# Kernel optimization log

Hardware: AMD Instinct MI355X
Metric: run time of the kernel (lower is better)

The kernel has to match this reference:

```python
import jax, jax.numpy as jnp
import numpy as np


def _ramp_filter(H):
    # skimage-style Fourier ramp filter: 2*|f| with f = fftfreq(H)
    f = np.fft.fftfreq(H)
    return (2.0 * np.abs(f)).astype(np.float32)


def setup_inputs() -> dict:
    key = jax.random.key(0)
    N, H_in, W_in, D_out = 8, 768, 360, 512
    radon_image = jax.random.normal(key, (N, 1, H_in, W_in), dtype=jnp.float32)
    hG = jnp.asarray(_ramp_filter(H_in)).reshape(1, 1, H_in, 1)
    return {"radon_image": radon_image, "hG": hG, "D_out": D_out}


def reference(radon_image, hG, D_out):
    N, _, H, W = radon_image.shape
    D = D_out
    # --- Fourier-domain ramp filtering (2D FFT, multiply by real filter along detector axis, real ifft) ---
    X = jnp.fft.fft2(radon_image[:, 0])                     # [N, H, W] complex
    h = hG[0, 0, :, 0]                                      # [H]
    filt = jnp.real(jnp.fft.ifft2(X * h[None, :, None])).astype(radon_image.dtype)  # [N, H, W]

    # --- backprojection grids (matches np.mgrid / tG construction) ---
    Xg, Yg = jnp.meshgrid(jnp.arange(D), jnp.arange(D), indexing="ij")
    xpr = (Xg - D // 2).astype(jnp.float32)
    ypr = (Yg - D // 2).astype(jnp.float32)
    th = (jnp.pi / 180.0) * jnp.linspace(0.0, 180.0, W, endpoint=False)  # [W]
    txs = -1.0 + jnp.arange(W, dtype=jnp.float32) * (2.0 / (W - 1))     # [W]

    hH = H // 2
    sy = (H - 1) / 2.0   # align_corners=True y scale
    sx = (W - 1) / 2.0   # align_corners=True x scale

    def body(recon, angle):
        th_i, tx_i = angle
        t = ypr * jnp.cos(th_i) - xpr * jnp.sin(th_i)       # [D, D]
        py = (t / hH + 1.0) * sy                            # pixel y coords [D, D]
        px = (tx_i + 1.0) * sx                              # scalar pixel x coord
        x0 = jnp.floor(px).astype(jnp.int32)
        wx = px - x0
        y0 = jnp.floor(py).astype(jnp.int32)
        wy = py - y0

        def samp_col(xi):
            vx = ((xi >= 0) & (xi < W)).astype(filt.dtype)
            col = filt[:, :, jnp.clip(xi, 0, W - 1)]        # [N, H]

            def samp_y(yi):
                vy = ((yi >= 0) & (yi < H)).astype(filt.dtype)
                return col[:, jnp.clip(yi, 0, H - 1)] * vy  # [N, D, D] zero-padded

            v = samp_y(y0) * (1.0 - wy) + samp_y(y0 + 1) * wy
            return v * vx

        val = samp_col(x0) * (1.0 - wx) + samp_col(x0 + 1) * wx  # [N, D, D]
        return recon + val, None

    recon0 = jnp.zeros((N, D, D), dtype=radon_image.dtype)
    recon, _ = jax.lax.scan(body, recon0, (th, txs))
    return (recon * (jnp.pi / (2.0 * W)))[:, None]          # [N, 1, D, D]
```

## Files before the change

kernel.cpp:

```cpp
#include <hip/hip_runtime.h>
#include <math.h>

#define N_IMG 8
#define H 768
#define W 360
#define D 512
#define SY 383.5f
#define SC 0.00436332312998582394f
#define NC 24
#define IPAD 384

typedef __fp16 h2 __attribute__((ext_vector_type(2)));
struct H2X2 { h2 a, b; };
typedef short short8 __attribute__((ext_vector_type(8)));
typedef float f32x4 __attribute__((ext_vector_type(4)));

__device__ inline unsigned bf16pair(float a, float b) {
    unsigned ua = __builtin_bit_cast(unsigned, a);
    unsigned ub = __builtin_bit_cast(unsigned, b);
    ua += 0x7FFFu + ((ua >> 16) & 1u);
    ub += 0x7FFFu + ((ub >> 16) & 1u);
    return (ua >> 16) | (ub & 0xFFFF0000u);
}

__global__ void build_g_kernel(const float* __restrict__ hG, float* __restrict__ g) {
    int m = blockIdx.x;
    int lane = threadIdx.x;
    float s = 0.f;
#pragma unroll
    for (int q = 0; q < 12; ++q) {
        int k = lane + 64 * q;
        int prod = (k * m) % H;
        float angr = (float)prod * 0.00818123086872313911f;
        s += hG[k] * cosf(angr);
    }
#pragma unroll
    for (int off = 32; off > 0; off >>= 1) s += __shfl_down(s, off);
    if (lane == 0) g[m] = s * (1.0f / (float)H);
}

#define KSTEPS 10

__global__ void build_angbg_kernel(const float* __restrict__ g, uint4* __restrict__ Bg,
                                   float2* __restrict__ ang) {
    int b = blockIdx.x;
    int t = threadIdx.x;
    if (b < 40) {
        int idx = b * 64 + t;
        int L  = idx & 63;
        int tj = idx >> 6;
        int nn = (tj & 3) * 16 + (L & 15);
        int kb = (tj >> 2) * 32 + (L >> 4) * 8;
        float bf[8];
#pragma unroll
        for (int s = 0; s < 8; ++s) {
            int d = nn + 128 - (kb + s);
            d += (d < 0) ? H : 0;
            bf[s] = g[d];
        }
        Bg[idx] = (uint4){bf16pair(bf[0], bf[1]), bf16pair(bf[2], bf[3]),
                          bf16pair(bf[4], bf[5]), bf16pair(bf[6], bf[7])};
    } else {
#pragma unroll
        for (int q = 0; q < 6; ++q) {
            int i = t + 64 * q;
            if (i < W) {
                float th = (float)i * 0.00872664625997164788f;
                float r = SY / 384.0f;
                ang[i] = make_float2(cosf(th) * r, -sinf(th) * r);
            }
        }
    }
}

__global__ __launch_bounds__(256)
void build_rc_kernel(const float* __restrict__ radon, uint4* __restrict__ rcC,
                     float4* __restrict__ out4) {
    __shared__ float xs[32][65];

    const int i0 = blockIdx.x * 64;
    const int c  = blockIdx.y;
    const int n  = blockIdx.z;
    const int tid = threadIdx.x;

    {
        int flat = ((n * NC) + c) * 6 + blockIdx.x;
        if (flat < 1024) {
            out4[flat * 512 + tid]       = make_float4(0.f, 0.f, 0.f, 0.f);
            out4[flat * 512 + 256 + tid] = make_float4(0.f, 0.f, 0.f, 0.f);
        }
    }

    {
        int mr    = tid >> 3;
        int lane8 = tid & 7;
        int ib = i0 + lane8 * 8;
        const float* src = radon + ((size_t)n * H + 32 * c + mr) * W + ib;
        float4 v0, v1;
        if (ib + 7 < W) {
            v0 = *(const float4*)src;
            v1 = *(const float4*)(src + 4);
        } else {
            v0 = make_float4(0.f, 0.f, 0.f, 0.f);
            v1 = make_float4(0.f, 0.f, 0.f, 0.f);
        }
        *(float4*)&xs[mr][lane8 * 8]     = v0;
        *(float4*)&xs[mr][lane8 * 8 + 4] = v1;
    }
    __syncthreads();

    const int il  = tid >> 2;
    const int oct = tid & 3;
    float v[8];
#pragma unroll
    for (int s = 0; s < 8; ++s) v[s] = xs[oct * 8 + s][il];
    uint4 pk = {bf16pair(v[0], v[1]), bf16pair(v[2], v[3]),
                bf16pair(v[4], v[5]), bf16pair(v[6], v[7])};
    rcC[(((size_t)n * NC + c) * IPAD + i0 + il) * 4 + oct] = pk;
}

__global__ __launch_bounds__(256)
void filt_gemm_kernel(const uint4* __restrict__ rcC, const uint4* __restrict__ Bg,
                      unsigned short* __restrict__ colp) {
    __shared__ _Float16 lx[16][64][4];

    const int grp = blockIdx.z;
    const int i0 = blockIdx.y * 16;
    const int y0 = blockIdx.x * 64;
    const int wv = threadIdx.x >> 6;
    const int L  = threadIdx.x & 63;

    const int c0 = (y0 / 32 + 20) % NC;
    const uint4* An = rcC + (size_t)(grp * 4 + wv) * NC * IPAD * 4;
    const int arow = i0 + (L & 15);
    const int aoff = L >> 4;

    f32x4 acc[4];
#pragma unroll
    for (int j = 0; j < 4; ++j) acc[j] = (f32x4){0.f, 0.f, 0.f, 0.f};

    for (int t = 0; t < KSTEPS; ++t) {
        int c = c0 + t;
        c -= (c >= NC) ? NC : 0;
        short8 a = __builtin_bit_cast(short8, An[((size_t)c * IPAD + arow) * 4 + aoff]);
#pragma unroll
        for (int j = 0; j < 4; ++j) {
            short8 b = __builtin_bit_cast(short8, Bg[(t * 4 + j) * 64 + L]);
            acc[j] = __builtin_amdgcn_mfma_f32_16x16x32_bf16(a, b, acc[j], 0, 0, 0);
        }
    }

#pragma unroll
    for (int j = 0; j < 4; ++j) {
#pragma unroll
        for (int r = 0; r < 4; ++r) {
            int ilc = (L >> 4) * 4 + r;
            int ylc = j * 16 + (L & 15);
            lx[ilc][ylc][wv] = (_Float16)(acc[j][r] * SC);
        }
    }
    __syncthreads();

    unsigned short* cp = colp + (size_t)grp * W * H * 4;
#pragma unroll
    for (int k = 0; k < 4; ++k) {
        int e = threadIdx.x + k * 256;
        int ilc = e >> 6, ylc = e & 63;
        int ig = i0 + ilc;
        if (ig < W) {
            uint2 v = *(const uint2*)&lx[ilc][ylc][0];
            *(uint2*)&cp[((size_t)ig * H + y0 + ylc) * 4] = v;
        }
    }
}

__global__ __launch_bounds__(512, 8)
void backproj_kernel(const unsigned short* __restrict__ colp,
                     const float2* __restrict__ angv, float* __restrict__ outb) {
    __shared__ __align__(16) H2X2 colh[2][H];

    const int bid = blockIdx.x;
    const int bz  = bid & 7;
    const int tle = bid >> 3;
    const int g  = bz >> 2;
    const int aq = bz & 3;
    const int a0 = aq * (W / 4);
    const int u0 = (tle >> 3) * 32;
    const int v0 = (tle & 7) * 64;
    const int tid = threadIdx.x;
    const int lane = tid & 63;
    const int tu = tid >> 6;

    const float vf = (float)(v0 + lane - D / 2);
    float uf[4];
#pragma unroll
    for (int r = 0; r < 4; ++r) uf[r] = (float)(u0 + tu + 8 * r - D / 2);

    const h2 hz = {(__fp16)0.f, (__fp16)0.f};
    float acc[4][4];
    h2 haccA[4], haccB[4];
#pragma unroll
    for (int r = 0; r < 4; ++r) {
#pragma unroll
        for (int nn = 0; nn < 4; ++nn) acc[r][nn] = 0.f;
        haccA[r] = hz;
        haccB[r] = hz;
    }

    const uint2* cp = (const uint2*)colp + (size_t)g * W * H;

    const int y1 = tid;
    const int y2 = tid + 512;

    {
        const int ab = a0 * H;
        colh[0][y1] = __builtin_bit_cast(H2X2, cp[ab + y1]);
        if (tid < 256) colh[0][y2] = __builtin_bit_cast(H2X2, cp[ab + y2]);
    }
    __syncthreads();

    for (int j = 0; j < W / 4; ++j) {
        int a = a0 + j;
        int an = (j + 1 < W / 4) ? (a + 1) : a;
        const int ab = an * H;
        uint2 d = cp[ab + y1];
        uint2 e = make_uint2(0u, 0u);
        if (tid < 256) e = cp[ab + y2];

        const int cb2 = j & 1;
        float2 AB = angv[a];
        float base = fmaf(vf, AB.x, SY);
#pragma unroll
        for (int r = 0; r < 4; ++r) {
            float py = fmaf(uf[r], AB.y, base);
            float wy = __builtin_amdgcn_fractf(py);
            int iy = (int)py;
            uint2 lo_raw = *(const uint2*)&colh[cb2][iy];
            uint2 hi_raw = *(const uint2*)&colh[cb2][iy + 1];
            H2X2 lo = __builtin_bit_cast(H2X2, lo_raw);
            H2X2 hi = __builtin_bit_cast(H2X2, hi_raw);
            h2 wy2 = __builtin_amdgcn_cvt_pkrtz(wy, wy);
            haccA[r] += lo.a + wy2 * (hi.a - lo.a);
            haccB[r] += lo.b + wy2 * (hi.b - lo.b);
        }

        if ((j & 15) == 15) {
#pragma unroll
            for (int r = 0; r < 4; ++r) {
                acc[r][0] += (float)haccA[r].x;
                acc[r][1] += (float)haccA[r].y;
                acc[r][2] += (float)haccB[r].x;
                acc[r][3] += (float)haccB[r].y;
                haccA[r] = hz;
                haccB[r] = hz;
            }
        }

        colh[cb2 ^ 1][y1] = __builtin_bit_cast(H2X2, d);
        if (tid < 256) colh[cb2 ^ 1][y2] = __builtin_bit_cast(H2X2, e);
        __syncthreads();
    }

#pragma unroll
    for (int r = 0; r < 4; ++r) {
        acc[r][0] += (float)haccA[r].x;
        acc[r][1] += (float)haccA[r].y;
        acc[r][2] += (float)haccB[r].x;
        acc[r][3] += (float)haccB[r].y;
        int u = u0 + tu + 8 * r;
#pragma unroll
        for (int nn = 0; nn < 4; ++nn) {
            size_t idx = ((size_t)(g * 4 + nn) * D + u) * D + v0 + lane;
            atomicAdd(&outb[idx], acc[r][nn]);
        }
    }
}

extern "C" void kernel_launch(void* const* d_in, const int* in_sizes, int n_in,
                              void* d_out, int out_size, void* d_ws, size_t ws_size,
                              hipStream_t stream) {
    const float* radon = (const float*)d_in[0];
    const float* hG    = (const float*)d_in[1];
    float* out = (float*)d_out;

    float*  g    = (float*)d_ws;
    float2* ang  = (float2*)((char*)d_ws + 4096);
    uint4*  Bg   = (uint4*)((char*)d_ws + 8192);
    unsigned short* colp = (unsigned short*)((char*)d_ws + 65536);
    uint4*  rcC  = (uint4*)((char*)d_ws + 4489216);

    build_g_kernel<<<H, 64, 0, stream>>>(hG, g);
    build_angbg_kernel<<<41, 64, 0, stream>>>(g, Bg, ang);
    build_rc_kernel<<<dim3(6, NC, N_IMG), 256, 0, stream>>>(radon, rcC, (float4*)out);
    filt_gemm_kernel<<<dim3(H / 64, 23, 2), 256, 0, stream>>>(rcC, Bg, colp);
    backproj_kernel<<<1024, 512, 0, stream>>>(colp, ang, out);
}
```

Before: 167.7 us.

## Interleave all 8 images per detector sample and split angles 8 ways in backprojection

The filtered sinogram layout changes from two groups of 4 images to a single interleaved 8-image row (16 bytes per detector bin), and the backprojection now processes all 8 images per block while splitting the angle range into 8 chunks instead of 4 images × 4 angle chunks. Each LDS lookup and bilinear weight computation is shared across 8 images rather than 4, which halves the per-image address/weight arithmetic and LDS instruction count. The cost is doubled LDS footprint (24 KB per block), more accumulator registers, a lowered occupancy hint (6 blocks), and twice as many atomic adds per block.

```diff
diff --git a/kernel.cpp b/kernel.cpp
--- a/kernel.cpp
+++ b/kernel.cpp
@@ -11,7 +11,6 @@
 #define IPAD 384
 
 typedef __fp16 h2 __attribute__((ext_vector_type(2)));
-struct H2X2 { h2 a, b; };
 typedef short short8 __attribute__((ext_vector_type(8)));
 typedef float f32x4 __attribute__((ext_vector_type(4)));
 
@@ -161,7 +160,6 @@
     }
     __syncthreads();
 
-    unsigned short* cp = colp + (size_t)grp * W * H * 4;
 #pragma unroll
     for (int k = 0; k < 4; ++k) {
         int e = threadIdx.x + k * 256;
@@ -169,22 +167,20 @@
         int ig = i0 + ilc;
         if (ig < W) {
             uint2 v = *(const uint2*)&lx[ilc][ylc][0];
-            *(uint2*)&cp[((size_t)ig * H + y0 + ylc) * 4] = v;
-        }
-    }
-}
-
-__global__ __launch_bounds__(512, 8)
-void backproj_kernel(const unsigned short* __restrict__ colp,
+            *(uint2*)&colp[((size_t)ig * H + y0 + ylc) * 8 + grp * 4] = v;
+        }
+    }
+}
+
+__global__ __launch_bounds__(512, 6)
+void backproj_kernel(const uint4* __restrict__ colp8,
                      const float2* __restrict__ angv, float* __restrict__ outb) {
-    __shared__ __align__(16) H2X2 colh[2][H];
+    __shared__ __align__(16) uint4 colh[2][H];
 
     const int bid = blockIdx.x;
-    const int bz  = bid & 7;
+    const int aq  = bid & 7;
     const int tle = bid >> 3;
-    const int g  = bz >> 2;
-    const int aq = bz & 3;
-    const int a0 = aq * (W / 4);
+    const int a0 = aq * (W / 8);
     const int u0 = (tle >> 3) * 32;
     const int v0 = (tle & 7) * 64;
     const int tid = threadIdx.x;
@@ -197,35 +193,33 @@
     for (int r = 0; r < 4; ++r) uf[r] = (float)(u0 + tu + 8 * r - D / 2);
 
     const h2 hz = {(__fp16)0.f, (__fp16)0.f};
-    float acc[4][4];
-    h2 haccA[4], haccB[4];
+    float acc[4][8];
+    h2 hacc[4][4];
 #pragma unroll
     for (int r = 0; r < 4; ++r) {
 #pragma unroll
-        for (int nn = 0; nn < 4; ++nn) acc[r][nn] = 0.f;
-        haccA[r] = hz;
-        haccB[r] = hz;
-    }
-
-    const uint2* cp = (const uint2*)colp + (size_t)g * W * H;
+        for (int nn = 0; nn < 8; ++nn) acc[r][nn] = 0.f;
+#pragma unroll
+        for (int p = 0; p < 4; ++p) hacc[r][p] = hz;
+    }
 
     const int y1 = tid;
     const int y2 = tid + 512;
 
     {
-        const int ab = a0 * H;
-        colh[0][y1] = __builtin_bit_cast(H2X2, cp[ab + y1]);
-        if (tid < 256) colh[0][y2] = __builtin_bit_cast(H2X2, cp[ab + y2]);
+        const size_t ab = (size_t)a0 * H;
+        colh[0][y1] = colp8[ab + y1];
+        if (tid < 256) colh[0][y2] = colp8[ab + y2];
     }
     __syncthreads();
 
-    for (int j = 0; j < W / 4; ++j) {
+    for (int j = 0; j < W / 8; ++j) {
         int a = a0 + j;
-        int an = (j + 1 < W / 4) ? (a + 1) : a;
-        const int ab = an * H;
-        uint2 d = cp[ab + y1];
-        uint2 e = make_uint2(0u, 0u);
-        if (tid < 256) e = cp[ab + y2];
+        int an = (j + 1 < W / 8) ? (a + 1) : a;
+        const size_t ab = (size_t)an * H;
+        uint4 d = colp8[ab + y1];
+        uint4 e = make_uint4(0u, 0u, 0u, 0u);
+        if (tid < 256) e = colp8[ab + y2];
 
         const int cb2 = j & 1;
         float2 AB = angv[a];
@@ -235,42 +229,55 @@
             float py = fmaf(uf[r], AB.y, base);
             float wy = __builtin_amdgcn_fractf(py);
             int iy = (int)py;
-            uint2 lo_raw = *(const uint2*)&colh[cb2][iy];
-            uint2 hi_raw = *(const uint2*)&colh[cb2][iy + 1];
-            H2X2 lo = __builtin_bit_cast(H2X2, lo_raw);
-            H2X2 hi = __builtin_bit_cast(H2X2, hi_raw);
+            uint4 lo4 = colh[cb2][iy];
+            uint4 hi4 = colh[cb2][iy + 1];
             h2 wy2 = __builtin_amdgcn_cvt_pkrtz(wy, wy);
-            haccA[r] += lo.a + wy2 * (hi.a - lo.a);
-            haccB[r] += lo.b + wy2 * (hi.b - lo.b);
+            {
+                h2 lo = __builtin_bit_cast(h2, lo4.x), hi = __builtin_bit_cast(h2, hi4.x);
+                hacc[r][0] += lo + wy2 * (hi - lo);
+            }
+            {
+                h2 lo = __builtin_bit_cast(h2, lo4.y), hi = __builtin_bit_cast(h2, hi4.y);
+                hacc[r][1] += lo + wy2 * (hi - lo);
+            }
+            {
+                h2 lo = __builtin_bit_cast(h2, lo4.z), hi = __builtin_bit_cast(h2, hi4.z);
+                hacc[r][2] += lo + wy2 * (hi - lo);
+            }
+            {
+                h2 lo = __builtin_bit_cast(h2, lo4.w), hi = __builtin_bit_cast(h2, hi4.w);
+                hacc[r][3] += lo + wy2 * (hi - lo);
+            }
         }
 
         if ((j & 15) == 15) {
 #pragma unroll
             for (int r = 0; r < 4; ++r) {
-                acc[r][0] += (float)haccA[r].x;
-                acc[r][1] += (float)haccA[r].y;
-                acc[r][2] += (float)haccB[r].x;
-                acc[r][3] += (float)haccB[r].y;
-                haccA[r] = hz;
-                haccB[r] = hz;
-            }
-        }
-
-        colh[cb2 ^ 1][y1] = __builtin_bit_cast(H2X2, d);
-        if (tid < 256) colh[cb2 ^ 1][y2] = __builtin_bit_cast(H2X2, e);
+#pragma unroll
+                for (int p = 0; p < 4; ++p) {
+                    acc[r][2 * p]     += (float)hacc[r][p].x;
+                    acc[r][2 * p + 1] += (float)hacc[r][p].y;
+                    hacc[r][p] = hz;
+                }
+            }
+        }
+
+        colh[cb2 ^ 1][y1] = d;
+        if (tid < 256) colh[cb2 ^ 1][y2] = e;
         __syncthreads();
     }
 
 #pragma unroll
     for (int r = 0; r < 4; ++r) {
-        acc[r][0] += (float)haccA[r].x;
-        acc[r][1] += (float)haccA[r].y;
-        acc[r][2] += (float)haccB[r].x;
-        acc[r][3] += (float)haccB[r].y;
+#pragma unroll
+        for (int p = 0; p < 4; ++p) {
+            acc[r][2 * p]     += (float)hacc[r][p].x;
+            acc[r][2 * p + 1] += (float)hacc[r][p].y;
+        }
         int u = u0 + tu + 8 * r;
 #pragma unroll
-        for (int nn = 0; nn < 4; ++nn) {
-            size_t idx = ((size_t)(g * 4 + nn) * D + u) * D + v0 + lane;
+        for (int nn = 0; nn < 8; ++nn) {
+            size_t idx = ((size_t)nn * D + u) * D + v0 + lane;
             atomicAdd(&outb[idx], acc[r][nn]);
         }
     }
@@ -293,5 +300,5 @@
     build_angbg_kernel<<<41, 64, 0, stream>>>(g, Bg, ang);
     build_rc_kernel<<<dim3(6, NC, N_IMG), 256, 0, stream>>>(radon, rcC, (float4*)out);
     filt_gemm_kernel<<<dim3(H / 64, 23, 2), 256, 0, stream>>>(rcC, Bg, colp);
-    backproj_kernel<<<1024, 512, 0, stream>>>(colp, ang, out);
-}
+    backproj_kernel<<<1024, 512, 0, stream>>>((const uint4*)colp, ang, out);
+}
```

New measurement: 168.3 us. About the same (+0.4%).
